# Performance work log

Hardware: AMD Instinct MI355X
Metric: run time of the kernel (lower is better)

The kernel has to match this reference:

```python
import jax, jax.numpy as jnp
import numpy as np


def _max_pairwise_dist(l, r):
    # l: [N, d], r: [M, d]
    # squared distances via Gram trick: ||l||^2 + ||r||^2 - 2 l.r  -> [N, M]
    l_sq = jnp.sum(l * l, axis=-1)  # [N]
    r_sq = jnp.sum(r * r, axis=-1)  # [M]
    cross = jnp.einsum('nd,md->nm', l, r)  # [N, M]
    sq_dists = l_sq[:, None] + r_sq[None, :] - 2.0 * cross
    sq_dists = jnp.maximum(sq_dists, 0.0)  # guard tiny negatives
    return jnp.sqrt(jnp.max(sq_dists))  # sqrt of max == max of sqrt (monotone)


def setup_inputs() -> dict:
    key = jax.random.key(0)
    k1, k2 = jax.random.split(key)
    N, M, D = 8192, 8192, 64
    return {
        'l_dfa_embeddings': jax.random.normal(k1, (N, D), dtype=jnp.float32),
        'r_dfa_embeddings': jax.random.normal(k2, (M, D), dtype=jnp.float32),
    }


def reference(l_dfa_embeddings, r_dfa_embeddings):
    # Max over all pairwise L2 distances between l and r state embeddings
    return _max_pairwise_dist(l_dfa_embeddings, r_dfa_embeddings)
```

## Files before the change

### kernel.cpp

```cpp
#include <hip/hip_runtime.h>
#include <hip/hip_bf16.h>
#include <math.h>


typedef __attribute__((ext_vector_type(8)))  short  short8;
typedef __attribute__((ext_vector_type(4)))  float  f32x4;
typedef __attribute__((ext_vector_type(16))) float  f32x16;

constexpr int D  = 64;
constexpr int NR = 8192;

__device__ __forceinline__ short f2bf(float f) {
    __hip_bfloat16 h = __float2bfloat16(f);
    return __builtin_bit_cast(short, h);
}


__global__ __launch_bounds__(256) void prepack_kernel(
    const float* __restrict__ L, const float* __restrict__ R,
    short* __restrict__ Apk, short* __restrict__ Bpk,
    float* __restrict__ lsq, float* __restrict__ rsq,
    unsigned int* __restrict__ outbits)
{
    const int t = blockIdx.x * 256 + threadIdx.x;
    const int r = t >> 2;
    const int j = t & 3;
    const bool isL = (r < NR);
    const int rr = isL ? r : r - NR;

    const float* src = (isL ? L : R) + (size_t)rr * D + j * 16;
    short* pk = isL ? Apk : Bpk;

    f32x4 v0 = *reinterpret_cast<const f32x4*>(src + 0);
    f32x4 v1 = *reinterpret_cast<const f32x4*>(src + 4);
    f32x4 v2 = *reinterpret_cast<const f32x4*>(src + 8);
    f32x4 v3 = *reinterpret_cast<const f32x4*>(src + 12);

    float p = 0.f;
    #pragma unroll
    for (int e = 0; e < 4; ++e) {
        p = fmaf(v0[e], v0[e], p); p = fmaf(v1[e], v1[e], p);
        p = fmaf(v2[e], v2[e], p); p = fmaf(v3[e], v3[e], p);
    }

    short8 w0, w1;
    #pragma unroll
    for (int e = 0; e < 4; ++e) {
        w0[e] = f2bf(v0[e]); w0[4+e] = f2bf(v1[e]);
        w1[e] = f2bf(v2[e]); w1[4+e] = f2bf(v3[e]);
    }
    const size_t base = ((size_t)(rr >> 5) * 4 + j) * 512;
    *reinterpret_cast<short8*>(pk + base + (0*32 + (rr & 31)) * 8) = w0;
    *reinterpret_cast<short8*>(pk + base + (1*32 + (rr & 31)) * 8) = w1;

    p += __shfl_xor(p, 1, 64);
    p += __shfl_xor(p, 2, 64);
    if (j == 0) (isL ? lsq : rsq)[rr] = p;

    if (t == 0) *outbits = 0u;
}

__global__ __launch_bounds__(256, 2) void pairdist_mfma_kernel(
    const short* __restrict__ Apk, const short* __restrict__ Bpk,
    const float* __restrict__ lsq, const float* __restrict__ rsq,
    unsigned int* __restrict__ outbits)
{
    __shared__ __align__(16) short A_lds[2][4][4][64][8];
    __shared__ __align__(16) float lsq_s[512];
    __shared__ __align__(16) float rsq_s[256];
    __shared__ float wmax_s[4];

    const int tid  = threadIdx.x;
    const int lane = tid & 63;
    const int wave = tid >> 6;
    const int xc = blockIdx.x;
    const int yb = blockIdx.y;

    const size_t Abase = (size_t)(xc * 16) * 2048;

    {
        const short* At = Apk + Abase;
        short* dst = &A_lds[0][0][0][0][0];
        #pragma unroll
        for (int i = 0; i < 4; ++i) {
            const int off = (i * 4 + wave) * 512;
            __builtin_amdgcn_global_load_lds(
                (const __attribute__((address_space(1))) unsigned int*)(At + off + lane * 8),
                (__attribute__((address_space(3))) unsigned int*)(dst + off),
                16, 0, 0);
        }
    }

    lsq_s[tid]       = lsq[xc * 512 + tid];
    lsq_s[256 + tid] = lsq[xc * 512 + 256 + tid];
    rsq_s[tid]       = rsq[yb * 256 + tid];

    const int wm = wave >> 1;
    const int wn = wave & 1;
    short8 bf[4][4];
    #pragma unroll
    for (int nj = 0; nj < 4; ++nj)
        #pragma unroll
        for (int kk = 0; kk < 4; ++kk)
            bf[nj][kk] = *reinterpret_cast<const short8*>(
                Bpk + ((size_t)(yb * 8 + wn * 4 + nj) * 4 + kk) * 512 + lane * 8);

    __syncthreads();

    const int col = lane & 31;
    const int h   = lane >> 5;
    float rq[4];
    #pragma unroll
    for (int nj = 0; nj < 4; ++nj) rq[nj] = rsq_s[wn * 128 + nj * 32 + col];

    float lmax = 0.f;
    int cur = 0;
    for (int t = 0; t < 4; ++t) {
        if (t < 3) {
            const short* At = Apk + Abase + (size_t)(t + 1) * 8192;
            short* dst = &A_lds[cur ^ 1][0][0][0][0];
            #pragma unroll
            for (int i = 0; i < 4; ++i) {
                const int off = (i * 4 + wave) * 512;
                __builtin_amdgcn_global_load_lds(
                    (const __attribute__((address_space(1))) unsigned int*)(At + off + lane * 8),
                    (__attribute__((address_space(3))) unsigned int*)(dst + off),
                    16, 0, 0);
            }
        }

        f32x16 acc[2][4] = {};
        #pragma unroll
        for (int kk = 0; kk < 4; ++kk) {
            short8 a0 = *reinterpret_cast<const short8*>(&A_lds[cur][wm*2+0][kk][lane][0]);
            short8 a1 = *reinterpret_cast<const short8*>(&A_lds[cur][wm*2+1][kk][lane][0]);
            #pragma unroll
            for (int nj = 0; nj < 4; ++nj) {
                acc[0][nj] = __builtin_amdgcn_mfma_f32_32x32x16_bf16(a0, bf[nj][kk], acc[0][nj], 0, 0, 0);
                acc[1][nj] = __builtin_amdgcn_mfma_f32_32x32x16_bf16(a1, bf[nj][kk], acc[1][nj], 0, 0, 0);
            }
        }

        #pragma unroll
        for (int mi = 0; mi < 2; ++mi) {
            const int rbase = t * 128 + (wm * 2 + mi) * 32 + 4 * h;
            f32x4 lq[4];
            lq[0] = *reinterpret_cast<const f32x4*>(&lsq_s[rbase +  0]);
            lq[1] = *reinterpret_cast<const f32x4*>(&lsq_s[rbase +  8]);
            lq[2] = *reinterpret_cast<const f32x4*>(&lsq_s[rbase + 16]);
            lq[3] = *reinterpret_cast<const f32x4*>(&lsq_s[rbase + 24]);
            #pragma unroll
            for (int nj = 0; nj < 4; ++nj) {
                float x[16];
                #pragma unroll
                for (int g = 0; g < 4; ++g)
                    #pragma unroll
                    for (int e = 0; e < 4; ++e)
                        x[g*4+e] = fmaf(-2.f, acc[mi][nj][g*4+e], lq[g][e]);
                float y0 = fmaxf(x[0],  x[1]),  y1 = fmaxf(x[2],  x[3]);
                float y2 = fmaxf(x[4],  x[5]),  y3 = fmaxf(x[6],  x[7]);
                float y4 = fmaxf(x[8],  x[9]),  y5 = fmaxf(x[10], x[11]);
                float y6 = fmaxf(x[12], x[13]), y7 = fmaxf(x[14], x[15]);
                float z0 = fmaxf(y0, y1), z1 = fmaxf(y2, y3);
                float z2 = fmaxf(y4, y5), z3 = fmaxf(y6, y7);
                float m  = fmaxf(fmaxf(z0, z1), fmaxf(z2, z3));
                lmax = fmaxf(lmax, m + rq[nj]);
            }
        }

        __syncthreads();
        cur ^= 1;
    }

    #pragma unroll
    for (int off = 32; off >= 1; off >>= 1)
        lmax = fmaxf(lmax, __shfl_xor(lmax, off, 64));
    if (lane == 0) wmax_s[wave] = lmax;
    __syncthreads();
    if (tid == 0) {
        float bmax = fmaxf(fmaxf(wmax_s[0], wmax_s[1]), fmaxf(wmax_s[2], wmax_s[3]));
        bmax = sqrtf(fmaxf(bmax, 0.f));
        atomicMax(outbits, __float_as_uint(bmax));
    }
}

extern "C" void kernel_launch(void* const* d_in, const int* in_sizes, int n_in,
                              void* d_out, int out_size, void* d_ws, size_t ws_size,
                              hipStream_t stream) {
    const float* L = (const float*)d_in[0];
    const float* R = (const float*)d_in[1];

    short* Apk = (short*)d_ws;
    short* Bpk = Apk + (size_t)NR * D;
    float* lsqg = (float*)(Bpk + (size_t)NR * D);
    float* rsqg = lsqg + NR;
    unsigned int* outbits = (unsigned int*)d_out;

    prepack_kernel<<<(2 * NR * 4) / 256, 256, 0, stream>>>(L, R, Apk, Bpk, lsqg, rsqg, outbits);
    pairdist_mfma_kernel<<<dim3(16, 32), dim3(256), 0, stream>>>(Apk, Bpk, lsqg, rsqg, outbits);
}
```

Before: 23.93 us.

## Move half of B fragments to LDS, split prepack finer, replace atomic with finalize kernel

The main kernel now keeps only two of the four B fragments in registers and stages the other two in shared memory through global_load_lds, which lowers VGPR pressure at the cost of extra LDS reads per k-step. The prepack kernel runs eight threads per row instead of four, so each thread handles one 8-element chunk. The per-block atomicMax is replaced by a slot array plus a third single-block finalize kernel that does the max and sqrt. A sched_barrier is added after the prefetch issue. The extra kernel launch adds fixed overhead.

After: 21.87 us. 8.6% less time.

```diff
diff --git a/kernel.cpp b/kernel.cpp
--- a/kernel.cpp
+++ b/kernel.cpp
@@ -9,6 +9,7 @@
 
 constexpr int D  = 64;
 constexpr int NR = 8192;
+constexpr int NBLK = 16 * 32;
 
 __device__ __forceinline__ short f2bf(float f) {
     __hip_bfloat16 h = __float2bfloat16(f);
@@ -19,53 +20,44 @@
 __global__ __launch_bounds__(256) void prepack_kernel(
     const float* __restrict__ L, const float* __restrict__ R,
     short* __restrict__ Apk, short* __restrict__ Bpk,
-    float* __restrict__ lsq, float* __restrict__ rsq,
-    unsigned int* __restrict__ outbits)
+    float* __restrict__ lsq, float* __restrict__ rsq)
 {
     const int t = blockIdx.x * 256 + threadIdx.x;
-    const int r = t >> 2;
-    const int j = t & 3;
+    const int r = t >> 3;
+    const int j = t & 7;
+    const int kk = j >> 1, kh = j & 1;
     const bool isL = (r < NR);
     const int rr = isL ? r : r - NR;
 
-    const float* src = (isL ? L : R) + (size_t)rr * D + j * 16;
+    const float* src = (isL ? L : R) + (size_t)rr * D + j * 8;
     short* pk = isL ? Apk : Bpk;
 
     f32x4 v0 = *reinterpret_cast<const f32x4*>(src + 0);
     f32x4 v1 = *reinterpret_cast<const f32x4*>(src + 4);
-    f32x4 v2 = *reinterpret_cast<const f32x4*>(src + 8);
-    f32x4 v3 = *reinterpret_cast<const f32x4*>(src + 12);
 
     float p = 0.f;
     #pragma unroll
-    for (int e = 0; e < 4; ++e) {
-        p = fmaf(v0[e], v0[e], p); p = fmaf(v1[e], v1[e], p);
-        p = fmaf(v2[e], v2[e], p); p = fmaf(v3[e], v3[e], p);
-    }
-
-    short8 w0, w1;
-    #pragma unroll
-    for (int e = 0; e < 4; ++e) {
-        w0[e] = f2bf(v0[e]); w0[4+e] = f2bf(v1[e]);
-        w1[e] = f2bf(v2[e]); w1[4+e] = f2bf(v3[e]);
-    }
-    const size_t base = ((size_t)(rr >> 5) * 4 + j) * 512;
-    *reinterpret_cast<short8*>(pk + base + (0*32 + (rr & 31)) * 8) = w0;
-    *reinterpret_cast<short8*>(pk + base + (1*32 + (rr & 31)) * 8) = w1;
+    for (int e = 0; e < 4; ++e) { p = fmaf(v0[e], v0[e], p); p = fmaf(v1[e], v1[e], p); }
+
+    short8 w;
+    #pragma unroll
+    for (int e = 0; e < 4; ++e) { w[e] = f2bf(v0[e]); w[4+e] = f2bf(v1[e]); }
+    *reinterpret_cast<short8*>(
+        pk + ((size_t)(rr >> 5) * 4 + kk) * 512 + (kh * 32 + (rr & 31)) * 8) = w;
 
     p += __shfl_xor(p, 1, 64);
     p += __shfl_xor(p, 2, 64);
+    p += __shfl_xor(p, 4, 64);
     if (j == 0) (isL ? lsq : rsq)[rr] = p;
-
-    if (t == 0) *outbits = 0u;
 }
 
 __global__ __launch_bounds__(256, 2) void pairdist_mfma_kernel(
     const short* __restrict__ Apk, const short* __restrict__ Bpk,
     const float* __restrict__ lsq, const float* __restrict__ rsq,
-    unsigned int* __restrict__ outbits)
+    float* __restrict__ slots)
 {
     __shared__ __align__(16) short A_lds[2][4][4][64][8];
+    __shared__ __align__(16) short B_lds[4][4][64][8];
     __shared__ __align__(16) float lsq_s[512];
     __shared__ __align__(16) float rsq_s[256];
     __shared__ float wmax_s[4];
@@ -80,13 +72,24 @@
 
     {
         const short* At = Apk + Abase;
-        short* dst = &A_lds[0][0][0][0][0];
-        #pragma unroll
-        for (int i = 0; i < 4; ++i) {
-            const int off = (i * 4 + wave) * 512;
+        #pragma unroll
+        for (int i = 0; i < 4; ++i)
             __builtin_amdgcn_global_load_lds(
-                (const __attribute__((address_space(1))) unsigned int*)(At + off + lane * 8),
-                (__attribute__((address_space(3))) unsigned int*)(dst + off),
+                (const __attribute__((address_space(1))) unsigned int*)
+                    (At + ((size_t)i * 4 + wave) * 512 + lane * 8),
+                (__attribute__((address_space(3))) unsigned int*)
+                    (&A_lds[0][i][wave][0][0]),
+                16, 0, 0);
+    }
+    {
+        #pragma unroll
+        for (int s = 0; s < 4; ++s) {
+            const int gsrc = yb * 8 + (s >> 1) * 4 + 2 + (s & 1);
+            __builtin_amdgcn_global_load_lds(
+                (const __attribute__((address_space(1))) unsigned int*)
+                    (Bpk + ((size_t)gsrc * 4 + wave) * 512 + lane * 8),
+                (__attribute__((address_space(3))) unsigned int*)
+                    (&B_lds[s][wave][0][0]),
                 16, 0, 0);
         }
     }
@@ -97,9 +100,9 @@
 
     const int wm = wave >> 1;
     const int wn = wave & 1;
-    short8 bf[4][4];
-    #pragma unroll
-    for (int nj = 0; nj < 4; ++nj)
+    short8 bf[2][4];
+    #pragma unroll
+    for (int nj = 0; nj < 2; ++nj)
         #pragma unroll
         for (int kk = 0; kk < 4; ++kk)
             bf[nj][kk] = *reinterpret_cast<const short8*>(
@@ -118,15 +121,15 @@
     for (int t = 0; t < 4; ++t) {
         if (t < 3) {
             const short* At = Apk + Abase + (size_t)(t + 1) * 8192;
-            short* dst = &A_lds[cur ^ 1][0][0][0][0];
             #pragma unroll
-            for (int i = 0; i < 4; ++i) {
-                const int off = (i * 4 + wave) * 512;
+            for (int i = 0; i < 4; ++i)
                 __builtin_amdgcn_global_load_lds(
-                    (const __attribute__((address_space(1))) unsigned int*)(At + off + lane * 8),
-                    (__attribute__((address_space(3))) unsigned int*)(dst + off),
+                    (const __attribute__((address_space(1))) unsigned int*)
+                        (At + ((size_t)i * 4 + wave) * 512 + lane * 8),
+                    (__attribute__((address_space(3))) unsigned int*)
+                        (&A_lds[cur ^ 1][i][wave][0][0]),
                     16, 0, 0);
-            }
+            __builtin_amdgcn_sched_barrier(0);
         }
 
         f32x16 acc[2][4] = {};
@@ -134,11 +137,16 @@
         for (int kk = 0; kk < 4; ++kk) {
             short8 a0 = *reinterpret_cast<const short8*>(&A_lds[cur][wm*2+0][kk][lane][0]);
             short8 a1 = *reinterpret_cast<const short8*>(&A_lds[cur][wm*2+1][kk][lane][0]);
-            #pragma unroll
-            for (int nj = 0; nj < 4; ++nj) {
-                acc[0][nj] = __builtin_amdgcn_mfma_f32_32x32x16_bf16(a0, bf[nj][kk], acc[0][nj], 0, 0, 0);
-                acc[1][nj] = __builtin_amdgcn_mfma_f32_32x32x16_bf16(a1, bf[nj][kk], acc[1][nj], 0, 0, 0);
-            }
+            short8 b2 = *reinterpret_cast<const short8*>(&B_lds[wn*2+0][kk][lane][0]);
+            short8 b3 = *reinterpret_cast<const short8*>(&B_lds[wn*2+1][kk][lane][0]);
+            acc[0][0] = __builtin_amdgcn_mfma_f32_32x32x16_bf16(a0, bf[0][kk], acc[0][0], 0, 0, 0);
+            acc[0][1] = __builtin_amdgcn_mfma_f32_32x32x16_bf16(a0, bf[1][kk], acc[0][1], 0, 0, 0);
+            acc[0][2] = __builtin_amdgcn_mfma_f32_32x32x16_bf16(a0, b2,        acc[0][2], 0, 0, 0);
+            acc[0][3] = __builtin_amdgcn_mfma_f32_32x32x16_bf16(a0, b3,        acc[0][3], 0, 0, 0);
+            acc[1][0] = __builtin_amdgcn_mfma_f32_32x32x16_bf16(a1, bf[0][kk], acc[1][0], 0, 0, 0);
+            acc[1][1] = __builtin_amdgcn_mfma_f32_32x32x16_bf16(a1, bf[1][kk], acc[1][1], 0, 0, 0);
+            acc[1][2] = __builtin_amdgcn_mfma_f32_32x32x16_bf16(a1, b2,        acc[1][2], 0, 0, 0);
+            acc[1][3] = __builtin_amdgcn_mfma_f32_32x32x16_bf16(a1, b3,        acc[1][3], 0, 0, 0);
         }
 
         #pragma unroll
@@ -179,8 +187,26 @@
     __syncthreads();
     if (tid == 0) {
         float bmax = fmaxf(fmaxf(wmax_s[0], wmax_s[1]), fmaxf(wmax_s[2], wmax_s[3]));
-        bmax = sqrtf(fmaxf(bmax, 0.f));
-        atomicMax(outbits, __float_as_uint(bmax));
+        slots[blockIdx.y * gridDim.x + blockIdx.x] = fmaxf(bmax, 0.f);
+    }
+}
+
+__global__ __launch_bounds__(512) void finalize_kernel(
+    const float* __restrict__ slots, float* __restrict__ out)
+{
+    __shared__ float wred[8];
+    const int tid = threadIdx.x;
+    float v = slots[tid];
+    #pragma unroll
+    for (int off = 32; off >= 1; off >>= 1)
+        v = fmaxf(v, __shfl_xor(v, off, 64));
+    if ((tid & 63) == 0) wred[tid >> 6] = v;
+    __syncthreads();
+    if (tid == 0) {
+        float m = wred[0];
+        #pragma unroll
+        for (int i = 1; i < 8; ++i) m = fmaxf(m, wred[i]);
+        out[0] = sqrtf(m);
     }
 }
 
@@ -194,8 +220,9 @@
     short* Bpk = Apk + (size_t)NR * D;
     float* lsqg = (float*)(Bpk + (size_t)NR * D);
     float* rsqg = lsqg + NR;
-    unsigned int* outbits = (unsigned int*)d_out;
-
-    prepack_kernel<<<(2 * NR * 4) / 256, 256, 0, stream>>>(L, R, Apk, Bpk, lsqg, rsqg, outbits);
-    pairdist_mfma_kernel<<<dim3(16, 32), dim3(256), 0, stream>>>(Apk, Bpk, lsqg, rsqg, outbits);
-}
+    float* slots = rsqg + NR;
+
+    prepack_kernel<<<(2 * NR * 8) / 256, 256, 0, stream>>>(L, R, Apk, Bpk, lsqg, rsqg);
+    pairdist_mfma_kernel<<<dim3(16, 32), dim3(256), 0, stream>>>(Apk, Bpk, lsqg, rsqg, slots);
+    finalize_kernel<<<1, 512, 0, stream>>>(slots, (float*)d_out);
+}
```
